# Optimization experiments

Measured on AMD Instinct MI355X. Metric: run time of the kernel, lower is better.

## Reference

```python
import jax, jax.numpy as jnp
import numpy as np

# The torch module's per-item while-loop repeatedly does masked argmin + mask
# update. That greedy extraction is mathematically a stable sort of the valid
# (unmasked) entries by time (stable argsort reproduces argmin's lowest-index
# tie-breaking), with positions past the valid count filled with pad_value.

def setup_inputs() -> dict:
    key = jax.random.key(0)
    k1, k2 = jax.random.split(key)
    B, L = 4096, 2048
    time = jax.random.uniform(k1, (B, L), dtype=jnp.float32)
    mask = jax.random.randint(k2, (B, L), 0, 2).astype(jnp.bool_)  # True = already visited / excluded
    pad_value = L  # sentinel index used to pad unpredicted slots
    return {"time": time, "mask": mask, "pad_value": pad_value}


def reference(time, mask, pad_value):
    # time: [B, L] float32, mask: [B, L] bool (True = excluded)
    B, L = time.shape
    # Masked entries pushed past every valid entry (original uses 1e6 fill,
    # but masked entries are never emitted since the loop stops at msk.all();
    # +inf preserves that invariant for the sorted formulation).
    keys = jnp.where(mask, jnp.inf, time)
    order = jnp.argsort(keys, axis=-1)               # stable: ties -> lowest index, same as argmin
    valid = jnp.sum(~mask, axis=-1)                  # [B] number of emitted indices per item
    pos = jnp.arange(L, dtype=valid.dtype)[None, :]  # [1, L]
    pred = jnp.where(pos < valid[:, None], order, pad_value)  # [B, L]
    return pred.astype(jnp.int32), valid.astype(jnp.int32)
```

## Files before the change

kernel.cpp:

```cpp
#include <hip/hip_runtime.h>
#include <stdint.h>

#define LROW 2048
#define THREADS 256
#define NBINS 1024
#define BPT (NBINS / THREADS)

__device__ __forceinline__ int swz(int b) {
    return ((b & (BPT - 1)) << 8) + (b >> 2);
}

__global__ __launch_bounds__(THREADS) void time_greedy_bucket_kernel(
    const float* __restrict__ time,
    const int* __restrict__ mask,
    const int* __restrict__ pad_value_p,
    int* __restrict__ pred,
    int* __restrict__ valid_out)
{
    __shared__ uint64_t keys[LROW];
    __shared__ uint32_t hist[NBINS];
    __shared__ uint32_t wsum[4];

    const int row = blockIdx.x;
    const int tid = threadIdx.x;
    const int lane = tid & 63;
    const int wid = tid >> 6;

#pragma unroll
    for (int e = 0; e < BPT; ++e) hist[tid + e * THREADS] = 0;
    __syncthreads();

    const float4* trow4 = (const float4*)(time + (size_t)row * LROW);
    const int4*   mrow4 = (const int4*)(mask + (size_t)row * LROW);

    uint32_t ukey[8];
    int      bkt[8];
    int      mval[8];
#pragma unroll
    for (int c = 0; c < 2; ++c) {
        const int v = tid + c * THREADS;
        const float4 tq = trow4[v];
        const int4   mq = mrow4[v];
        const float tf[4] = {tq.x, tq.y, tq.z, tq.w};
        const int   mf[4] = {mq.x, mq.y, mq.z, mq.w};
#pragma unroll
        for (int j = 0; j < 4; ++j) {
            const int e = c * 4 + j;
            const uint32_t fb = __float_as_uint(tf[j]);
            ukey[e] = fb ^ ((uint32_t)((int32_t)fb >> 31) | 0x80000000u);
            int b = (int)(tf[j] * (float)NBINS);
            b = (b < 0) ? 0 : ((b > NBINS - 1) ? NBINS - 1 : b);
            bkt[e] = b;
            mval[e] = mf[j];
            if (!mf[j]) atomicAdd(&hist[swz(b)], 1u);
        }
    }
    __syncthreads();

    uint32_t h[BPT];
    uint32_t lsum = 0;
#pragma unroll
    for (int e = 0; e < BPT; ++e) {
        h[e] = hist[e * THREADS + tid];
        lsum += h[e];
    }
    uint32_t incl = lsum;
#pragma unroll
    for (int off = 1; off < 64; off <<= 1) {
        const uint32_t y = __shfl_up(incl, off, 64);
        if (lane >= off) incl += y;
    }
    if (lane == 63) wsum[wid] = incl;
    __syncthreads();
    uint32_t woff = 0, total = 0;
#pragma unroll
    for (int w = 0; w < 4; ++w) {
        const uint32_t s = wsum[w];
        if (w < wid) woff += s;
        total += s;
    }
    uint32_t run = woff + incl - lsum;
#pragma unroll
    for (int e = 0; e < BPT; ++e) {
        hist[e * THREADS + tid] = run;
        run += h[e];
    }
    __syncthreads();

#pragma unroll
    for (int c = 0; c < 2; ++c) {
#pragma unroll
        for (int j = 0; j < 4; ++j) {
            const int e = c * 4 + j;
            if (!mval[e]) {
                const int i = 4 * tid + c * (4 * THREADS) + j;
                const uint32_t pos = atomicAdd(&hist[swz(bkt[e])], 1u);
                keys[pos] = ((uint64_t)ukey[e] << 32) | (uint32_t)i;
            }
        }
    }
    __syncthreads();

#pragma unroll
    for (int e = 0; e < BPT; ++e) {
        const int b = BPT * tid + e;
        const uint32_t start = (b == 0) ? 0u : hist[swz(b - 1)];
        const uint32_t end = hist[swz(b)];
        for (uint32_t i = start + 1; i < end; ++i) {
            const uint64_t v = keys[i];
            uint32_t j = i;
            while (j > start && keys[j - 1] > v) {
                keys[j] = keys[j - 1];
                --j;
            }
            keys[j] = v;
        }
    }
    __syncthreads();

    const int vld = (int)total;
    const int pad = pad_value_p[0];
    int* prow = pred + (size_t)row * LROW;
#pragma unroll
    for (int c = 0; c < LROW / THREADS; ++c) {
        const int i = tid + c * THREADS;
        const uint64_t k = keys[i];
        prow[i] = (i < vld) ? (int)(uint32_t)k : pad;
    }
    if (tid == 0) valid_out[row] = vld;
}

extern "C" void kernel_launch(void* const* d_in, const int* in_sizes, int n_in,
                              void* d_out, int out_size, void* d_ws, size_t ws_size,
                              hipStream_t stream) {
    const float* time = (const float*)d_in[0];
    const int* mask = (const int*)d_in[1];
    const int* pad_value = (const int*)d_in[2];

    const int B = in_sizes[0] / LROW;

    int* pred = (int*)d_out;
    int* valid_out = pred + (size_t)B * LROW;

    time_greedy_bucket_kernel<<<B, THREADS, 0, stream>>>(time, mask, pad_value,
                                                         pred, valid_out);
}
```

Before: 113.7 us.

## Replace per-bucket insertion sort with per-element rank counting and scatter

```diff
diff --git a/kernel.cpp b/kernel.cpp
--- a/kernel.cpp
+++ b/kernel.cpp
@@ -10,7 +10,7 @@
     return ((b & (BPT - 1)) << 8) + (b >> 2);
 }
 
-__global__ __launch_bounds__(THREADS) void time_greedy_bucket_kernel(
+__global__ __launch_bounds__(THREADS) void time_greedy_rank_kernel(
     const float* __restrict__ time,
     const int* __restrict__ mask,
     const int* __restrict__ pad_value_p,
@@ -18,7 +18,8 @@
     int* __restrict__ valid_out)
 {
     __shared__ uint64_t keys[LROW];
-    __shared__ uint32_t hist[NBINS];
+    __shared__ uint32_t hstart[NBINS];
+    __shared__ uint32_t hpos[NBINS];
     __shared__ uint32_t wsum[4];
 
     const int row = blockIdx.x;
@@ -27,7 +28,7 @@
     const int wid = tid >> 6;
 
 #pragma unroll
-    for (int e = 0; e < BPT; ++e) hist[tid + e * THREADS] = 0;
+    for (int e = 0; e < BPT; ++e) hpos[tid + e * THREADS] = 0;
     __syncthreads();
 
     const float4* trow4 = (const float4*)(time + (size_t)row * LROW);
@@ -52,7 +53,7 @@
             b = (b < 0) ? 0 : ((b > NBINS - 1) ? NBINS - 1 : b);
             bkt[e] = b;
             mval[e] = mf[j];
-            if (!mf[j]) atomicAdd(&hist[swz(b)], 1u);
+            if (!mf[j]) atomicAdd(&hpos[swz(b)], 1u);
         }
     }
     __syncthreads();
@@ -61,7 +62,7 @@
     uint32_t lsum = 0;
 #pragma unroll
     for (int e = 0; e < BPT; ++e) {
-        h[e] = hist[e * THREADS + tid];
+        h[e] = hpos[e * THREADS + tid];
         lsum += h[e];
     }
     uint32_t incl = lsum;
@@ -82,7 +83,8 @@
     uint32_t run = woff + incl - lsum;
 #pragma unroll
     for (int e = 0; e < BPT; ++e) {
-        hist[e * THREADS + tid] = run;
+        hstart[e * THREADS + tid] = run;
+        hpos[e * THREADS + tid] = run;
         run += h[e];
     }
     __syncthreads();
@@ -94,26 +96,9 @@
             const int e = c * 4 + j;
             if (!mval[e]) {
                 const int i = 4 * tid + c * (4 * THREADS) + j;
-                const uint32_t pos = atomicAdd(&hist[swz(bkt[e])], 1u);
+                const uint32_t pos = atomicAdd(&hpos[swz(bkt[e])], 1u);
                 keys[pos] = ((uint64_t)ukey[e] << 32) | (uint32_t)i;
             }
-        }
-    }
-    __syncthreads();
-
-#pragma unroll
-    for (int e = 0; e < BPT; ++e) {
-        const int b = BPT * tid + e;
-        const uint32_t start = (b == 0) ? 0u : hist[swz(b - 1)];
-        const uint32_t end = hist[swz(b)];
-        for (uint32_t i = start + 1; i < end; ++i) {
-            const uint64_t v = keys[i];
-            uint32_t j = i;
-            while (j > start && keys[j - 1] > v) {
-                keys[j] = keys[j - 1];
-                --j;
-            }
-            keys[j] = v;
         }
     }
     __syncthreads();
@@ -122,11 +107,25 @@
     const int pad = pad_value_p[0];
     int* prow = pred + (size_t)row * LROW;
 #pragma unroll
-    for (int c = 0; c < LROW / THREADS; ++c) {
-        const int i = tid + c * THREADS;
-        const uint64_t k = keys[i];
-        prow[i] = (i < vld) ? (int)(uint32_t)k : pad;
+    for (int c = 0; c < 2; ++c) {
+#pragma unroll
+        for (int j = 0; j < 4; ++j) {
+            const int e = c * 4 + j;
+            if (!mval[e]) {
+                const int i = 4 * tid + c * (4 * THREADS) + j;
+                const uint64_t my = ((uint64_t)ukey[e] << 32) | (uint32_t)i;
+                const int sb = swz(bkt[e]);
+                const uint32_t s = hstart[sb];
+                const uint32_t en = hpos[sb];
+                uint32_t rank = 0;
+                for (uint32_t q = s; q < en; ++q)
+                    rank += (keys[q] < my) ? 1u : 0u;
+                prow[s + rank] = i;
+            }
+        }
     }
+
+    for (int i = vld + tid; i < LROW; i += THREADS) prow[i] = pad;
     if (tid == 0) valid_out[row] = vld;
 }
 
@@ -142,6 +141,6 @@
     int* pred = (int*)d_out;
     int* valid_out = pred + (size_t)B * LROW;
 
-    time_greedy_bucket_kernel<<<B, THREADS, 0, stream>>>(time, mask, pad_value,
-                                                         pred, valid_out);
+    time_greedy_rank_kernel<<<B, THREADS, 0, stream>>>(time, mask, pad_value,
+                                                       pred, valid_out);
 }
```

Result: slower. 117.1 us (+3.0%).
